# Optimization experiments

Measured on AMD Instinct MI355X. Metric: run time of the kernel, lower is better.

Reference implementation:

```python
import jax, jax.numpy as jnp
import numpy as np

B, N, D = 4, 2048, 512      # batch, seq, dim_in
DK = DV = 512               # dim_k == dim_v (required by fc input width)
NH = 8
HK = DK // NH               # per-head dk == dv == 64
SCALE = 1.0 / np.sqrt(HK)
LN_EPS = 1e-5


def setup_inputs() -> dict:
    key = jax.random.key(0)
    ks = jax.random.split(key, 8)
    s = 0.02
    return {
        "x": jax.random.normal(ks[0], (B, N, D), dtype=jnp.float32),
        "Wq": jax.random.normal(ks[1], (D, DK), dtype=jnp.float32) * s,
        "Wk": jax.random.normal(ks[2], (D, DK), dtype=jnp.float32) * s,
        "Wv": jax.random.normal(ks[3], (D, DV), dtype=jnp.float32) * s,
        "Wf": jax.random.normal(ks[4], (2 * DK, D), dtype=jnp.float32) * s,
        "bf": jnp.zeros((D,), dtype=jnp.float32),
        "gamma": jnp.ones((D,), dtype=jnp.float32),
        "beta": jnp.zeros((D,), dtype=jnp.float32),
    }


def reference(x, Wq, Wk, Wv, Wf, bf, gamma, beta):
    b, n, _ = x.shape
    # projections -> [b, nh, n, hk]; q_c/q_f etc. are identical in the source,
    # so compute once.
    def proj(W):
        return jnp.einsum('bnd,dk->bnk', x, W).reshape(b, n, NH, -1).transpose(0, 2, 1, 3)
    q, k, v = proj(Wq), proj(Wk), proj(Wv)

    # conventional branch: softmax over n x n scores
    dist_c = jax.nn.softmax(jnp.einsum('bhqd,bhkd->bhqk', q, k) * SCALE, axis=-1)
    att_c = jnp.einsum('bhqk,bhkd->bhqd', dist_c, v)          # [b,nh,n,hk]
    att_c = att_c.transpose(0, 2, 1, 3).reshape(b, n, DV)

    # feature branch: softmax over dk x dk scores (linear-complexity variant)
    dist_f = jax.nn.softmax(jnp.einsum('bhnk,bhnq->bhkq', k, q) * SCALE, axis=-1)
    att_f = jnp.einsum('bhnd,bhdq->bhnq', v, dist_f)           # [b,nh,n,hk]
    att_f = att_f.transpose(0, 2, 1, 3).reshape(b, n, DV)

    att = jnp.concatenate([att_c, att_f], axis=2)              # [b,n,2*dk]
    out = jax.nn.relu(att @ Wf + bf)                           # dropout=eval (identity)
    out = out + x
    mu = jnp.mean(out, axis=-1, keepdims=True)
    var = jnp.var(out, axis=-1, keepdims=True)
    out = (out - mu) * jax.lax.rsqrt(var + LN_EPS) * gamma + beta
    return out
```

## Files before the change

### kernel.cpp

```cpp
#include <hip/hip_runtime.h>
#include <math.h>
#include <stdint.h>

#define B_   4
#define N_   2048
#define D_   512
#define DK_  512
#define NH_  8
#define HK_  64
#define LN_EPS_ 1e-5f
#define QS_  0.18033688011112042f

typedef unsigned short u16;
typedef __attribute__((ext_vector_type(8))) short short8;
typedef __attribute__((ext_vector_type(4))) float f32x4;
typedef __attribute__((ext_vector_type(8))) unsigned short u16x8;

__device__ __forceinline__ u16 f2bf(float x) {
    uint32_t u = __builtin_bit_cast(uint32_t, x);
    return (u16)((u + 0x7fffu + ((u >> 16) & 1u)) >> 16);
}
__device__ __forceinline__ u16 f2bf_fast(float x) {
    return (u16)((__builtin_bit_cast(uint32_t, x) + 0x8000u) >> 16);
}
__device__ __forceinline__ float b2f(u16 v) {
    return __builtin_bit_cast(float, (uint32_t)v << 16);
}
__device__ __forceinline__ uint32_t cvtpk_bf16(float lo, float hi) {
    uint32_t r;
    asm("v_cvt_pk_bf16_f32 %0, %1, %2" : "=v"(r) : "v"(lo), "v"(hi));
    return r;
}
__device__ __forceinline__ float exp2f_fast(float x) {
    return __builtin_amdgcn_exp2f(x);
}

__device__ __forceinline__ void gload16(const void* g, void* l) {
    __builtin_amdgcn_global_load_lds(
        reinterpret_cast<const __attribute__((address_space(1))) void*>(
            reinterpret_cast<uintptr_t>(g)),
        reinterpret_cast<__attribute__((address_space(3))) void*>(
            static_cast<uint32_t>(reinterpret_cast<uintptr_t>(l))),
        16, 0, 0);
}

__global__ __launch_bounds__(256) void prep_kernel(
    const float* __restrict__ x, const float* __restrict__ Wq,
    const float* __restrict__ Wk, const float* __restrict__ Wv,
    const float* __restrict__ Wf, u16* __restrict__ xb,
    u16* __restrict__ wqkvT, u16* __restrict__ wfT)
{
    __shared__ float t[32][33];
    const int bid = blockIdx.x, tid = threadIdx.x;
    if (bid < 2048) {
        const int i = (bid * 256 + tid) * 8;
        const float4 a = *reinterpret_cast<const float4*>(&x[i]);
        const float4 b = *reinterpret_cast<const float4*>(&x[i + 4]);
        u16x8 o;
        o[0] = f2bf(a.x); o[1] = f2bf(a.y); o[2] = f2bf(a.z); o[3] = f2bf(a.w);
        o[4] = f2bf(b.x); o[5] = f2bf(b.y); o[6] = f2bf(b.z); o[7] = f2bf(b.w);
        *reinterpret_cast<u16x8*>(&xb[i]) = o;
        return;
    }
    const float* W;
    u16* dst;
    int K, Nc, nt, kt;
    if (bid < 2816) {
        const int z = (bid - 2048) >> 8, rem = (bid - 2048) & 255;
        W = z == 0 ? Wq : (z == 1 ? Wk : Wv);
        dst = wqkvT + (size_t)z * 512 * 512;
        K = 512; Nc = 512;
        nt = (rem & 15) * 32; kt = (rem >> 4) * 32;
    } else {
        const int rem = bid - 2816;
        W = Wf; dst = wfT; K = 1024; Nc = 512;
        nt = (rem & 15) * 32; kt = (rem >> 4) * 32;
    }
    {
        const int r = tid >> 3, c0 = (tid & 7) * 4;
        const float4 v = *reinterpret_cast<const float4*>(
            &W[(size_t)(kt + r) * Nc + nt + c0]);
        t[r][c0] = v.x; t[r][c0 + 1] = v.y; t[r][c0 + 2] = v.z; t[r][c0 + 3] = v.w;
    }
    __syncthreads();
    {
        const int nidx = tid >> 3, kc = (tid & 7) * 4;
        u16 o[4];
        #pragma unroll
        for (int j = 0; j < 4; ++j) o[j] = f2bf(t[kc + j][nidx]);
        *reinterpret_cast<ushort4*>(&dst[(size_t)(nt + nidx) * K + kt + kc]) =
            make_ushort4(o[0], o[1], o[2], o[3]);
    }
}

__global__ __launch_bounds__(256) void gemm_qkv_kernel(
    const u16* __restrict__ A, const u16* __restrict__ Bt,
    u16* __restrict__ qb, u16* __restrict__ kb,
    u16* __restrict__ vb, u16* __restrict__ vt)
{
    __shared__ u16 As0[64 * 64], As1[64 * 64];
    __shared__ u16 Bs0[128 * 64], Bs1[128 * 64];
    const int tid = threadIdx.x;
    const int lane = tid & 63, wave = tid >> 6;
    const int wm = wave >> 1, wn = wave & 1;
    const int l15 = lane & 15, lg = lane >> 4;
    const int bid = ((int)blockIdx.x & 7) * 192 + ((int)blockIdx.x >> 3);
    const int nt = (bid % 12) * 128;
    const int mt = (bid / 12) * 64;

    f32x4 acc[2][4] = {};

#define QKV_STAGE(kt, AS, BS) do {                                             \
    _Pragma("unroll")                                                          \
    for (int i_ = 0; i_ < 2; ++i_) {                                           \
        const int ob_ = (wave * 2 + i_) * 1024;                                \
        const int o_ = ob_ + lane * 16;                                        \
        const int row_ = o_ >> 7;                                              \
        const int inner_ = (o_ & 127) ^ ((row_ & 7) << 4);                     \
        gload16((const char*)A + ((size_t)(mt + row_) * 512 + (kt) * 64) * 2   \
                    + inner_, (char*)(AS) + ob_);                              \
    }                                                                          \
    _Pragma("unroll")                                                          \
    for (int i_ = 0; i_ < 4; ++i_) {                                           \
        const int ob_ = (wave * 4 + i_) * 1024;                                \
        const int o_ = ob_ + lane * 16;                                        \
        const int row_ = o_ >> 7;                                              \
        const int inner_ = (o_ & 127) ^ ((row_ & 7) << 4);                     \
        gload16((const char*)Bt + ((size_t)(nt + row_) * 512 + (kt) * 64) * 2  \
                    + inner_, (char*)(BS) + ob_);                              \
    }                                                                          \
} while (0)

#define QKV_COMP(AS, BS) do {                                                  \
    _Pragma("unroll")                                                          \
    for (int ks = 0; ks < 2; ++ks) {                                           \
        const int kb2 = ks * 32 + lg * 8;                                      \
        short8 af[2], bfr[4];                                                  \
        _Pragma("unroll")                                                      \
        for (int mi = 0; mi < 2; ++mi) {                                       \
            const int r = wm * 32 + mi * 16 + l15;                             \
            af[mi] = *reinterpret_cast<const short8*>(                         \
                &(AS)[r * 64 + (kb2 ^ ((r & 7) << 3))]);                       \
        }                                                                      \
        _Pragma("unroll")                                                      \
        for (int ni = 0; ni < 4; ++ni) {                                       \
            const int r = wn * 64 + ni * 16 + l15;                             \
            bfr[ni] = *reinterpret_cast<const short8*>(                        \
                &(BS)[r * 64 + (kb2 ^ ((r & 7) << 3))]);                       \
        }                                                                      \
        _Pragma("unroll")                                                      \
        for (int mi = 0; mi < 2; ++mi)                                         \
            _Pragma("unroll")                                                  \
            for (int ni = 0; ni < 4; ++ni)                                     \
                acc[mi][ni] = __builtin_amdgcn_mfma_f32_16x16x32_bf16(         \
                    af[mi], bfr[ni], acc[mi][ni], 0, 0, 0);                    \
    }                                                                          \
} while (0)

    QKV_STAGE(0, As0, Bs0);
    __syncthreads();
    #pragma unroll 1
    for (int kt = 0; kt < 8; kt += 2) {
        QKV_STAGE(kt + 1, As1, Bs1);
        QKV_COMP(As0, Bs0);
        __syncthreads();
        if (kt + 2 < 8) QKV_STAGE(kt + 2, As0, Bs0);
        QKV_COMP(As1, Bs1);
        __syncthreads();
    }
#undef QKV_STAGE
#undef QKV_COMP

    #pragma unroll
    for (int mi = 0; mi < 2; ++mi) {
        #pragma unroll
        for (int ni = 0; ni < 4; ++ni) {
            const int col = nt + wn * 64 + ni * 16 + l15;
            const int row0 = mt + wm * 32 + mi * 16 + lg * 4;
            if (col < 512) {
                #pragma unroll
                for (int jj = 0; jj < 4; ++jj)
                    qb[(size_t)(row0 + jj) * 512 + col] =
                        f2bf(acc[mi][ni][jj] * QS_);
            } else if (col < 1024) {
                #pragma unroll
                for (int jj = 0; jj < 4; ++jj)
                    kb[(size_t)(row0 + jj) * 512 + col - 512] =
                        f2bf(acc[mi][ni][jj]);
            } else {
                const int dfull = col - 1024;
                const int hh = dfull >> 6, dd = dfull & 63;
                const int bb = row0 >> 11, nn = row0 & 2047;
                u16 o4[4];
                #pragma unroll
                for (int jj = 0; jj < 4; ++jj) {
                    o4[jj] = f2bf(acc[mi][ni][jj]);
                    vb[(size_t)(row0 + jj) * 512 + dfull] = o4[jj];
                }
                *reinterpret_cast<ushort4*>(
                    &vt[(((size_t)(bb * NH_ + hh)) * HK_ + dd) * N_ + nn]) =
                    make_ushort4(o4[0], o4[1], o4[2], o4[3]);
            }
        }
    }
}

__global__ __launch_bounds__(256) void gemm_fc_kernel(
    const u16* __restrict__ A, const u16* __restrict__ Bt,
    u16* __restrict__ C, const float* __restrict__ bias,
    const float* __restrict__ resid)
{
    __shared__ u16 As0[64 * 64], As1[64 * 64];
    __shared__ u16 Bs0[128 * 64], Bs1[128 * 64];
    const int tid = threadIdx.x;
    const int lane = tid & 63, wave = tid >> 6;
    const int wm = wave >> 1, wn = wave & 1;
    const int l15 = lane & 15, lg = lane >> 4;
    const int bid = ((int)blockIdx.x & 7) * 64 + ((int)blockIdx.x >> 3);
    const int nt = (bid & 3) * 128;
    const int mt = (bid >> 2) * 64;

    f32x4 acc[2][4] = {};

#define FC_STAGE(kt, AS, BS) do {                                              \
    _Pragma("unroll")                                                          \
    for (int i_ = 0; i_ < 2; ++i_) {                                           \
        const int ob_ = (wave * 2 + i_) * 1024;                                \
        const int o_ = ob_ + lane * 16;                                        \
        const int row_ = o_ >> 7;                                              \
        const int inner_ = (o_ & 127) ^ ((row_ & 7) << 4);                     \
        gload16((const char*)A + ((size_t)(mt + row_) * 1024 + (kt) * 64) * 2  \
                    + inner_, (char*)(AS) + ob_);                              \
    }                                                                          \
    _Pragma("unroll")                                                          \
    for (int i_ = 0; i_ < 4; ++i_) {                                           \
        const int ob_ = (wave * 4 + i_) * 1024;                                \
        const int o_ = ob_ + lane * 16;                                        \
        const int row_ = o_ >> 7;                                              \
        const int inner_ = (o_ & 127) ^ ((row_ & 7) << 4);                     \
        gload16((const char*)Bt + ((size_t)(nt + row_) * 1024 + (kt) * 64) * 2 \
                    + inner_, (char*)(BS) + ob_);                              \
    }                                                                          \
} while (0)

#define FC_COMP(AS, BS) do {                                                   \
    _Pragma("unroll")                                                          \
    for (int ks = 0; ks < 2; ++ks) {                                           \
        const int kb2 = ks * 32 + lg * 8;                                      \
        short8 af[2], bfr[4];                                                  \
        _Pragma("unroll")                                                      \
        for (int mi = 0; mi < 2; ++mi) {                                       \
            const int r = wm * 32 + mi * 16 + l15;                             \
            af[mi] = *reinterpret_cast<const short8*>(                         \
                &(AS)[r * 64 + (kb2 ^ ((r & 7) << 3))]);                       \
        }                                                                      \
        _Pragma("unroll")                                                      \
        for (int ni = 0; ni < 4; ++ni) {                                       \
            const int r = wn * 64 + ni * 16 + l15;                             \
            bfr[ni] = *reinterpret_cast<const short8*>(                        \
                &(BS)[r * 64 + (kb2 ^ ((r & 7) << 3))]);                       \
        }                                                                      \
        _Pragma("unroll")                                                      \
        for (int mi = 0; mi < 2; ++mi)                                         \
            _Pragma("unroll")                                                  \
            for (int ni = 0; ni < 4; ++ni)                                     \
                acc[mi][ni] = __builtin_amdgcn_mfma_f32_16x16x32_bf16(         \
                    af[mi], bfr[ni], acc[mi][ni], 0, 0, 0);                    \
    }                                                                          \
} while (0)

    FC_STAGE(0, As0, Bs0);
    __syncthreads();
    #pragma unroll 1
    for (int kt = 0; kt < 16; kt += 2) {
        FC_STAGE(kt + 1, As1, Bs1);
        FC_COMP(As0, Bs0);
        __syncthreads();
        if (kt + 2 < 16) FC_STAGE(kt + 2, As0, Bs0);
        FC_COMP(As1, Bs1);
        __syncthreads();
    }
#undef FC_STAGE
#undef FC_COMP

    #pragma unroll
    for (int mi = 0; mi < 2; ++mi) {
        #pragma unroll
        for (int ni = 0; ni < 4; ++ni) {
            const int col = nt + wn * 64 + ni * 16 + l15;
            const int row0 = mt + wm * 32 + mi * 16 + lg * 4;
            #pragma unroll
            for (int jj = 0; jj < 4; ++jj) {
                const size_t row = (size_t)(row0 + jj);
                float v = acc[mi][ni][jj];
                v += bias[col];
                v = fmaxf(v, 0.0f);
                v += resid[row * 512 + col];
                C[row * 512 + col] = f2bf(v);
            }
        }
    }
}

__global__ __launch_bounds__(256) void flash_featS_kernel(
    const u16* __restrict__ Qb, const u16* __restrict__ Kb,
    const u16* __restrict__ Vt, u16* __restrict__ att,
    float* __restrict__ partials)
{
    __shared__ u16 sh[24576];
    const int tid = threadIdx.x;
    const int lane = tid & 63, wave = tid >> 6;
    const int l15 = lane & 15, lg = lane >> 4;

    if ((int)blockIdx.x >= 512) {
        u16* KsT = sh;
        u16* QsT = sh + 4096;
        const int fid = (int)blockIdx.x - 512;
        const int ns = fid & 7, h = (fid >> 3) & 7, b = fid >> 6;
        const size_t hbase = (size_t)b * N_ * DK_ + (size_t)h * HK_;

        f32x4 acc[4] = {};
        for (int c = 0; c < 4; ++c) {
            const int n0 = ns * 256 + c * 64;
            __syncthreads();
            #pragma unroll
            for (int it = 0; it < 2; ++it) {
                const int idx = tid + it * 256;
                const int n = idx >> 3, d0 = (idx & 7) * 8;
                const u16x8 kv = *reinterpret_cast<const u16x8*>(
                    &Kb[hbase + (size_t)(n0 + n) * DK_ + d0]);
                const u16x8 qv = *reinterpret_cast<const u16x8*>(
                    &Qb[hbase + (size_t)(n0 + n) * DK_ + d0]);
                #pragma unroll
                for (int j = 0; j < 8; ++j) {
                    const int r = d0 + j;
                    const int cidx = n ^ ((r & 7) << 3);
                    KsT[r * 64 + cidx] = kv[j];
                    QsT[r * 64 + cidx] = qv[j];
                }
            }
            __syncthreads();
            #pragma unroll
            for (int ks = 0; ks < 2; ++ks) {
                const int kb2 = ks * 32 + lg * 8;
                const int ar = wave * 16 + l15;
                const short8 aK = *reinterpret_cast<const short8*>(
                    &KsT[ar * 64 + (kb2 ^ ((ar & 7) << 3))]);
                #pragma unroll
                for (int ni = 0; ni < 4; ++ni) {
                    const int br = ni * 16 + l15;
                    const short8 bQ = *reinterpret_cast<const short8*>(
                        &QsT[br * 64 + (kb2 ^ ((br & 7) << 3))]);
                    acc[ni] = __builtin_amdgcn_mfma_f32_16x16x32_bf16(
                        aK, bQ, acc[ni], 0, 0, 0);
                }
            }
        }
        const int bh = b * NH_ + h;
        #pragma unroll
        for (int ni = 0; ni < 4; ++ni)
            #pragma unroll
            for (int jj = 0; jj < 4; ++jj) {
                const int row = wave * 16 + lg * 4 + jj;
                partials[(((size_t)ns * 32 + bh) * 64 + row) * 64 + ni * 16 + l15] =
                    acc[ni][jj];
            }
        return;
    }

    u16* kb0 = sh;
    u16* kb1 = sh + 4096;
    u16* vb0 = sh + 8192;
    u16* vb1 = sh + 12288;
    u16* Ps  = sh + 16384;
    const int lbid = (((int)blockIdx.x & 7) << 6) + ((int)blockIdx.x >> 3);
    const int qt = lbid & 15, h = (lbid >> 4) & 7, b = lbid >> 7;

    short8 aq[2][2];
    #pragma unroll
    for (int qs = 0; qs < 2; ++qs) {
        const int qrow = qt * 128 + qs * 64 + wave * 16 + l15;
        const u16* qp = Qb + ((size_t)(b * N_ + qrow)) * DK_ + h * HK_ + lg * 8;
        aq[qs][0] = *reinterpret_cast<const short8*>(qp);
        aq[qs][1] = *reinterpret_cast<const short8*>(qp + 32);
    }
    short8 ones;
    #pragma unroll
    for (int i = 0; i < 8; ++i) ones[i] = (short)0x3F80;

    const u16* Kbase = Kb + (size_t)b * N_ * DK_ + (size_t)h * HK_;
    const u16* Vbase = Vt + ((size_t)(b * NH_ + h)) * HK_ * N_;
    unsigned long long* Ps64 = reinterpret_cast<unsigned long long*>(Ps);

    f32x4 o[2][5] = {};
    float m_[2] = {-1e30f, -1e30f};
    f32x4 SA[2][4], SB[2][4];

    const int ob0 = wave * 1024, oo0 = ob0 + lane * 16;
    const int row0s = oo0 >> 7;
    const int in0 = (oo0 & 127) ^ ((row0s & 7) << 4);

#define STAGE_K(ktile, KBUF) do {                                              \
    gload16((const char*)Kbase +                                               \
                ((size_t)((ktile) * 64 + row0s) * DK_) * 2 + in0,              \
            (char*)(KBUF) + ob0);                                              \
    gload16((const char*)Kbase +                                               \
                ((size_t)((ktile) * 64 + 32 + row0s) * DK_) * 2 + in0,         \
            (char*)(KBUF) + 4096 + ob0);                                       \
} while (0)

#define STAGE_V(ktile, VBUF) do {                                              \
    gload16((const char*)Vbase +                                               \
                ((size_t)row0s * N_ + (ktile) * 64) * 2 + in0,                 \
            (char*)(VBUF) + ob0);                                              \
    gload16((const char*)Vbase +                                               \
                ((size_t)(32 + row0s) * N_ + (ktile) * 64) * 2 + in0,          \
            (char*)(VBUF) + 4096 + ob0);                                       \
} while (0)

#define QK_STEP(S, KBUF) do {                                                  \
    _Pragma("unroll")                                                          \
    for (int qs = 0; qs < 2; ++qs)                                             \
        _Pragma("unroll")                                                      \
        for (int t = 0; t < 4; ++t)                                            \
            S[qs][t] = (f32x4){0.0f, 0.0f, 0.0f, 0.0f};                        \
    __builtin_amdgcn_s_setprio(1);                                             \
    _Pragma("unroll")                                                          \
    for (int ks = 0; ks < 2; ++ks) {                                           \
        const int kb2 = ks * 32 + lg * 8;                                      \
        _Pragma("unroll")                                                      \
        for (int t = 0; t < 4; ++t) {                                          \
            const int r = t * 16 + l15;                                        \
            const short8 bk = *reinterpret_cast<const short8*>(                \
                &(KBUF)[r * 64 + (kb2 ^ ((r & 7) << 3))]);                     \
            S[0][t] = __builtin_amdgcn_mfma_f32_16x16x32_bf16(                 \
                bk, aq[0][ks], S[0][t], 0, 0, 0);                              \
            S[1][t] = __builtin_amdgcn_mfma_f32_16x16x32_bf16(                 \
                bk, aq[1][ks], S[1][t], 0, 0, 0);                              \
        }                                                                      \
    }                                                                          \
    __builtin_amdgcn_s_setprio(0);                                             \
} while (0)

#define SMPV_STEP(S, VBUF) do {                                                \
    float rmax[2], cm;                                                         \
    _Pragma("unroll")                                                          \
    for (int qs = 0; qs < 2; ++qs) {                                           \
        float a0 = fmaxf(fmaxf(S[qs][0][0], S[qs][0][1]),                      \
                         fmaxf(S[qs][0][2], S[qs][0][3]));                     \
        float a1 = fmaxf(fmaxf(S[qs][1][0], S[qs][1][1]),                      \
                         fmaxf(S[qs][1][2], S[qs][1][3]));                     \
        float a2 = fmaxf(fmaxf(S[qs][2][0], S[qs][2][1]),                      \
                         fmaxf(S[qs][2][2], S[qs][2][3]));                     \
        float a3 = fmaxf(fmaxf(S[qs][3][0], S[qs][3][1]),                      \
                         fmaxf(S[qs][3][2], S[qs][3][3]));                     \
        rmax[qs] = fmaxf(fmaxf(a0, a1), fmaxf(a2, a3));                        \
    }                                                                          \
    cm = fmaxf(rmax[0] - m_[0], rmax[1] - m_[1]);                              \
    if (__any(cm > 8.0f)) {                                                    \
        _Pragma("unroll")                                                      \
        for (int qs = 0; qs < 2; ++qs) {                                       \
            float rm = rmax[qs];                                               \
            rm = fmaxf(rm, __shfl_xor(rm, 16));                                \
            rm = fmaxf(rm, __shfl_xor(rm, 32));                                \
            const float newm = fmaxf(m_[qs], rm);                              \
            const float fac = exp2f_fast(m_[qs] - newm);                       \
            m_[qs] = newm;                                                     \
            float facq[4];                                                     \
            _Pragma("unroll")                                                  \
            for (int jj = 0; jj < 4; ++jj)                                     \
                facq[jj] = __shfl(fac, lg * 4 + jj);                           \
            _Pragma("unroll")                                                  \
            for (int t = 0; t < 5; ++t)                                        \
                _Pragma("unroll")                                              \
                for (int jj = 0; jj < 4; ++jj)                                 \
                    o[qs][t][jj] *= facq[jj];                                  \
        }                                                                      \
    }                                                                          \
    _Pragma("unroll")                                                          \
    for (int qs = 0; qs < 2; ++qs) {                                           \
        const int prow = qs * 64 + wave * 16 + l15;                            \
        const int pb64 = prow * 16;                                            \
        const int sw1 = (prow & 7) << 1;                                       \
        _Pragma("unroll")                                                      \
        for (int t = 0; t < 4; ++t) {                                          \
            const float p0 = exp2f_fast(S[qs][t][0] - m_[qs]);                 \
            const float p1 = exp2f_fast(S[qs][t][1] - m_[qs]);                 \
            const float p2 = exp2f_fast(S[qs][t][2] - m_[qs]);                 \
            const float p3 = exp2f_fast(S[qs][t][3] - m_[qs]);                 \
            const uint32_t lo = cvtpk_bf16(p0, p1);                            \
            const uint32_t hi = cvtpk_bf16(p2, p3);                            \
            Ps64[pb64 + ((t * 4 + lg) ^ sw1)] =                                \
                (unsigned long long)lo | ((unsigned long long)hi << 32);       \
        }                                                                      \
    }                                                                          \
    __builtin_amdgcn_s_setprio(1);                                             \
    _Pragma("unroll")                                                          \
    for (int ks = 0; ks < 2; ++ks) {                                           \
        const int kb2 = ks * 32 + lg * 8;                                      \
        const int pr0 = wave * 16 + l15;                                       \
        const int pr1 = 64 + pr0;                                              \
        const short8 ap0 = *reinterpret_cast<const short8*>(                   \
            &Ps[pr0 * 64 + (kb2 ^ ((pr0 & 7) << 3))]);                         \
        const short8 ap1 = *reinterpret_cast<const short8*>(                   \
            &Ps[pr1 * 64 + (kb2 ^ ((pr1 & 7) << 3))]);                         \
        _Pragma("unroll")                                                      \
        for (int t = 0; t < 4; ++t) {                                          \
            const int dr = t * 16 + l15;                                       \
            const short8 bv = *reinterpret_cast<const short8*>(                \
                &(VBUF)[dr * 64 + (kb2 ^ ((dr & 7) << 3))]);                   \
            o[0][t] = __builtin_amdgcn_mfma_f32_16x16x32_bf16(                 \
                ap0, bv, o[0][t], 0, 0, 0);                                    \
            o[1][t] = __builtin_amdgcn_mfma_f32_16x16x32_bf16(                 \
                ap1, bv, o[1][t], 0, 0, 0);                                    \
        }                                                                      \
        o[0][4] = __builtin_amdgcn_mfma_f32_16x16x32_bf16(                     \
            ap0, ones, o[0][4], 0, 0, 0);                                      \
        o[1][4] = __builtin_amdgcn_mfma_f32_16x16x32_bf16(                     \
            ap1, ones, o[1][4], 0, 0, 0);                                      \
    }                                                                          \
    __builtin_amdgcn_s_setprio(0);                                             \
} while (0)

    STAGE_K(0, kb0);
    STAGE_K(1, kb1);
    STAGE_V(0, vb0);
    __syncthreads();
    QK_STEP(SA, kb0);

    #pragma unroll 1
    for (int t2 = 0; t2 < 30; t2 += 2) {
        __syncthreads();
        STAGE_K(t2 + 2, kb0);
        STAGE_V(t2 + 1, vb1);
        QK_STEP(SB, kb1);
        SMPV_STEP(SA, vb0);
        __syncthreads();
        STAGE_K(t2 + 3, kb1);
        STAGE_V(t2 + 2, vb0);
        QK_STEP(SA, kb0);
        SMPV_STEP(SB, vb1);
    }
    __syncthreads();
    STAGE_V(31, vb1);
    QK_STEP(SB, kb1);
    SMPV_STEP(SA, vb0);
    __syncthreads();
    SMPV_STEP(SB, vb1);

#undef STAGE_K
#undef STAGE_V
#undef QK_STEP
#undef SMPV_STEP

    #pragma unroll
    for (int qs = 0; qs < 2; ++qs)
        #pragma unroll
        for (int jj = 0; jj < 4; ++jj) {
            const float inv = 1.0f / o[qs][4][jj];
            const size_t row = (size_t)b * N_ + qt * 128 + qs * 64 + wave * 16 + lg * 4 + jj;
            #pragma unroll
            for (int t = 0; t < 4; ++t)
                att[row * (2 * DK_) + h * HK_ + t * 16 + l15] =
                    f2bf_fast(o[qs][t][jj] * inv);
        }
}

__global__ __launch_bounds__(256) void featSM_kernel(
    const float* __restrict__ partials, u16* __restrict__ distfT)
{
    const int bh = blockIdx.x, rg = blockIdx.y, tid = threadIdx.x;
    const int r = rg * 16 + (tid >> 4);
    const int tl = tid & 15;
    float v[4] = {0.0f, 0.0f, 0.0f, 0.0f};
    for (int s = 0; s < 8; ++s) {
        const float4 a = *reinterpret_cast<const float4*>(
            &partials[(((size_t)s * 32 + bh) * 64 + r) * 64 + tl * 4]);
        v[0] += a.x; v[1] += a.y; v[2] += a.z; v[3] += a.w;
    }
    float m = fmaxf(fmaxf(v[0], v[1]), fmaxf(v[2], v[3]));
    m = fmaxf(m, __shfl_xor(m, 1));
    m = fmaxf(m, __shfl_xor(m, 2));
    m = fmaxf(m, __shfl_xor(m, 4));
    m = fmaxf(m, __shfl_xor(m, 8));
    float sum = 0.0f;
    #pragma unroll
    for (int j = 0; j < 4; ++j) { v[j] = exp2f_fast(v[j] - m); sum += v[j]; }
    sum += __shfl_xor(sum, 1);
    sum += __shfl_xor(sum, 2);
    sum += __shfl_xor(sum, 4);
    sum += __shfl_xor(sum, 8);
    const float inv = 1.0f / sum;
    #pragma unroll
    for (int j = 0; j < 4; ++j)
        distfT[(size_t)bh * 4096 + (tl * 4 + j) * 64 + r] = f2bf_fast(v[j] * inv);
}

__global__ __launch_bounds__(256) void featAV_mfma(
    const u16* __restrict__ V, const u16* __restrict__ distfT,
    u16* __restrict__ att)
{
    __shared__ u16 Bs[64 * 64];
    __shared__ u16 As[64 * 64];
    const int tid = threadIdx.x;
    const int lane = tid & 63, wave = tid >> 6;
    const int l15 = lane & 15, lg = lane >> 4;
    const int ns = blockIdx.x, h = blockIdx.y, b = blockIdx.z;
    const int bh = b * NH_ + h;
    const int n0 = ns * 64;

    #pragma unroll
    for (int it = 0; it < 2; ++it) {
        const int idx = tid + it * 256;
        const int r = idx >> 3, c0 = (idx & 7) * 8;
        const u16x8 dv = *reinterpret_cast<const u16x8*>(
            &distfT[(size_t)bh * 4096 + r * 64 + c0]);
        *reinterpret_cast<u16x8*>(&Bs[r * 64 + (c0 ^ ((r & 7) << 3))]) = dv;
    }
    #pragma unroll
    for (int i = 0; i < 2; ++i) {
        const int ob = (wave * 2 + i) * 1024;
        const int o_ = ob + lane * 16;
        const int row = o_ >> 7;
        const int inner = (o_ & 127) ^ ((row & 7) << 4);
        gload16((const char*)V + ((size_t)(b * N_ + n0 + row) * DK_ + h * HK_) * 2 + inner,
                (char*)As + ob);
    }
    __syncthreads();
    f32x4 acc[4] = {};
    #pragma unroll
    for (int ks = 0; ks < 2; ++ks) {
        const int kb2 = ks * 32 + lg * 8;
        const int ar = wave * 16 + l15;
        const short8 av = *reinterpret_cast<const short8*>(
            &As[ar * 64 + (kb2 ^ ((ar & 7) << 3))]);
        #pragma unroll
        for (int ni = 0; ni < 4; ++ni) {
            const int br = ni * 16 + l15;
            const short8 bd = *reinterpret_cast<const short8*>(
                &Bs[br * 64 + (kb2 ^ ((br & 7) << 3))]);
            acc[ni] = __builtin_amdgcn_mfma_f32_16x16x32_bf16(av, bd, acc[ni], 0, 0, 0);
        }
    }
    #pragma unroll
    for (int ni = 0; ni < 4; ++ni)
        #pragma unroll
        for (int jj = 0; jj < 4; ++jj)
            att[((size_t)b * N_ + n0 + wave * 16 + lg * 4 + jj) * (2 * DK_)
                + 512 + h * HK_ + ni * 16 + l15] = f2bf_fast(acc[ni][jj]);
}

__global__ __launch_bounds__(256) void ln_kernel(
    const u16* __restrict__ fc, const float* __restrict__ gamma,
    const float* __restrict__ beta, float* __restrict__ out)
{
    const int row = blockIdx.x * 4 + (threadIdx.x >> 6);
    const int lane = threadIdx.x & 63;
    const int c = lane * 8;
    const u16x8 v = *reinterpret_cast<const u16x8*>(&fc[(size_t)row * D_ + c]);
    float f[8];
    float s = 0.0f, sq = 0.0f;
    #pragma unroll
    for (int j = 0; j < 8; ++j) {
        f[j] = b2f(v[j]);
        s += f[j];
        sq = fmaf(f[j], f[j], sq);
    }
    #pragma unroll
    for (int off = 32; off >= 1; off >>= 1) {
        s  += __shfl_xor(s, off);
        sq += __shfl_xor(sq, off);
    }
    const float mu = s * (1.0f / D_);
    const float var = sq * (1.0f / D_) - mu * mu;
    const float rstd = rsqrtf(var + LN_EPS_);
    const float4 g0 = *reinterpret_cast<const float4*>(&gamma[c]);
    const float4 g1 = *reinterpret_cast<const float4*>(&gamma[c + 4]);
    const float4 b0 = *reinterpret_cast<const float4*>(&beta[c]);
    const float4 b1 = *reinterpret_cast<const float4*>(&beta[c + 4]);
    const float gg[8] = {g0.x, g0.y, g0.z, g0.w, g1.x, g1.y, g1.z, g1.w};
    const float bb[8] = {b0.x, b0.y, b0.z, b0.w, b1.x, b1.y, b1.z, b1.w};
    float4 o0, o1;
    o0.x = (f[0] - mu) * rstd * gg[0] + bb[0];
    o0.y = (f[1] - mu) * rstd * gg[1] + bb[1];
    o0.z = (f[2] - mu) * rstd * gg[2] + bb[2];
    o0.w = (f[3] - mu) * rstd * gg[3] + bb[3];
    o1.x = (f[4] - mu) * rstd * gg[4] + bb[4];
    o1.y = (f[5] - mu) * rstd * gg[5] + bb[5];
    o1.z = (f[6] - mu) * rstd * gg[6] + bb[6];
    o1.w = (f[7] - mu) * rstd * gg[7] + bb[7];
    *reinterpret_cast<float4*>(&out[(size_t)row * D_ + c]) = o0;
    *reinterpret_cast<float4*>(&out[(size_t)row * D_ + c + 4]) = o1;
}

extern "C" void kernel_launch(void* const* d_in, const int* in_sizes, int n_in,
                              void* d_out, int out_size, void* d_ws, size_t ws_size,
                              hipStream_t stream)
{
    (void)in_sizes; (void)n_in; (void)out_size; (void)ws_size;
    const float* x     = (const float*)d_in[0];
    const float* Wq    = (const float*)d_in[1];
    const float* Wk    = (const float*)d_in[2];
    const float* Wv    = (const float*)d_in[3];
    const float* Wf    = (const float*)d_in[4];
    const float* bf    = (const float*)d_in[5];
    const float* gamma = (const float*)d_in[6];
    const float* beta  = (const float*)d_in[7];
    float* out = (float*)d_out;

    char* w = (char*)d_ws;
    const size_t SZE = (size_t)B_ * N_ * DK_;
    u16* xb     = (u16*)w;   w += SZE * 2;
    u16* wqkvT  = (u16*)w;   w += (size_t)1536 * 512 * 2;
    u16* wfT    = (u16*)w;   w += (size_t)512 * 1024 * 2;
    u16* qb     = (u16*)w;   w += SZE * 2;
    u16* kb     = (u16*)w;   w += SZE * 2;
    u16* vb     = (u16*)w;   w += SZE * 2;
    u16* vt     = (u16*)w;   w += SZE * 2;
    u16* attb   = (u16*)w;   w += SZE * 2 * 2;
    float* partials = (float*)w; w += (size_t)8 * 32 * 4096 * 4;
    u16* distfT = (u16*)w;   w += (size_t)32 * 4096 * 2;
    u16* fcout  = (u16*)w;

    const dim3 blk(256);

    prep_kernel<<<dim3(3328), blk, 0, stream>>>(x, Wq, Wk, Wv, Wf, xb, wqkvT, wfT);

    gemm_qkv_kernel<<<dim3(1536), blk, 0, stream>>>(xb, wqkvT, qb, kb, vb, vt);

    flash_featS_kernel<<<dim3(768), blk, 0, stream>>>(qb, kb, vt, attb, partials);

    featSM_kernel<<<dim3(32, 4), blk, 0, stream>>>(partials, distfT);
    featAV_mfma<<<dim3(32, NH_, B_), blk, 0, stream>>>(vb, distfT, attb);

    gemm_fc_kernel<<<dim3(512), blk, 0, stream>>>(attb, wfT, fcout, bf, x);

    ln_kernel<<<dim3(2048), blk, 0, stream>>>(fcout, gamma, beta, out);
}
```

Baseline: 116.3 us.

## Fuse x fp32-to-bf16 conversion into QKV GEMM and move Wf transpose into flash kernel

The QKV GEMM now loads fp32 x directly through registers, converts it to bf16 and writes it into swizzled LDS, so the separate x conversion pass and the xb buffer go away. The Wf transpose/convert blocks move out of the prep kernel and become extra blocks in the flash_featS launch, which shrinks prep to the QKV weight transposes only. This removes a full write and re-read of x in bf16, but the GEMM A operand now reads twice as many bytes through register-staged loads instead of direct global-to-LDS loads, and the conversion adds ALU work in the GEMM loop.

```diff
diff --git a/kernel.cpp b/kernel.cpp
--- a/kernel.cpp
+++ b/kernel.cpp
@@ -45,41 +45,19 @@
 }
 
 __global__ __launch_bounds__(256) void prep_kernel(
-    const float* __restrict__ x, const float* __restrict__ Wq,
-    const float* __restrict__ Wk, const float* __restrict__ Wv,
-    const float* __restrict__ Wf, u16* __restrict__ xb,
-    u16* __restrict__ wqkvT, u16* __restrict__ wfT)
+    const float* __restrict__ Wq, const float* __restrict__ Wk,
+    const float* __restrict__ Wv, u16* __restrict__ wqkvT)
 {
     __shared__ float t[32][33];
     const int bid = blockIdx.x, tid = threadIdx.x;
-    if (bid < 2048) {
-        const int i = (bid * 256 + tid) * 8;
-        const float4 a = *reinterpret_cast<const float4*>(&x[i]);
-        const float4 b = *reinterpret_cast<const float4*>(&x[i + 4]);
-        u16x8 o;
-        o[0] = f2bf(a.x); o[1] = f2bf(a.y); o[2] = f2bf(a.z); o[3] = f2bf(a.w);
-        o[4] = f2bf(b.x); o[5] = f2bf(b.y); o[6] = f2bf(b.z); o[7] = f2bf(b.w);
-        *reinterpret_cast<u16x8*>(&xb[i]) = o;
-        return;
-    }
-    const float* W;
-    u16* dst;
-    int K, Nc, nt, kt;
-    if (bid < 2816) {
-        const int z = (bid - 2048) >> 8, rem = (bid - 2048) & 255;
-        W = z == 0 ? Wq : (z == 1 ? Wk : Wv);
-        dst = wqkvT + (size_t)z * 512 * 512;
-        K = 512; Nc = 512;
-        nt = (rem & 15) * 32; kt = (rem >> 4) * 32;
-    } else {
-        const int rem = bid - 2816;
-        W = Wf; dst = wfT; K = 1024; Nc = 512;
-        nt = (rem & 15) * 32; kt = (rem >> 4) * 32;
-    }
+    const int z = bid >> 8, rem = bid & 255;
+    const float* W = z == 0 ? Wq : (z == 1 ? Wk : Wv);
+    u16* dst = wqkvT + (size_t)z * 512 * 512;
+    const int nt = (rem & 15) * 32, kt = (rem >> 4) * 32;
     {
         const int r = tid >> 3, c0 = (tid & 7) * 4;
         const float4 v = *reinterpret_cast<const float4*>(
-            &W[(size_t)(kt + r) * Nc + nt + c0]);
+            &W[(size_t)(kt + r) * 512 + nt + c0]);
         t[r][c0] = v.x; t[r][c0 + 1] = v.y; t[r][c0 + 2] = v.z; t[r][c0 + 3] = v.w;
     }
     __syncthreads();
@@ -88,13 +66,13 @@
         u16 o[4];
         #pragma unroll
         for (int j = 0; j < 4; ++j) o[j] = f2bf(t[kc + j][nidx]);
-        *reinterpret_cast<ushort4*>(&dst[(size_t)(nt + nidx) * K + kt + kc]) =
+        *reinterpret_cast<ushort4*>(&dst[(size_t)(nt + nidx) * 512 + kt + kc]) =
             make_ushort4(o[0], o[1], o[2], o[3]);
     }
 }
 
 __global__ __launch_bounds__(256) void gemm_qkv_kernel(
-    const u16* __restrict__ A, const u16* __restrict__ Bt,
+    const float* __restrict__ X, const u16* __restrict__ Bt,
     u16* __restrict__ qb, u16* __restrict__ kb,
     u16* __restrict__ vb, u16* __restrict__ vt)
 {
@@ -108,18 +86,38 @@
     const int nt = (bid % 12) * 128;
     const int mt = (bid / 12) * 64;
 
+    const int ar_ = tid >> 2;
+    const int ac0_ = (tid & 3) * 16;
+    const int aswz_ = (ar_ & 7) << 4;
+    float4 al0, al1, al2, al3;
+
     f32x4 acc[2][4] = {};
 
-#define QKV_STAGE(kt, AS, BS) do {                                             \
-    _Pragma("unroll")                                                          \
-    for (int i_ = 0; i_ < 2; ++i_) {                                           \
-        const int ob_ = (wave * 2 + i_) * 1024;                                \
-        const int o_ = ob_ + lane * 16;                                        \
-        const int row_ = o_ >> 7;                                              \
-        const int inner_ = (o_ & 127) ^ ((row_ & 7) << 4);                     \
-        gload16((const char*)A + ((size_t)(mt + row_) * 512 + (kt) * 64) * 2   \
-                    + inner_, (char*)(AS) + ob_);                              \
-    }                                                                          \
+#define A_LOAD(kt) do {                                                        \
+    const float* xp_ = &X[(size_t)(mt + ar_) * 512 + (kt) * 64 + ac0_];        \
+    al0 = *reinterpret_cast<const float4*>(xp_);                               \
+    al1 = *reinterpret_cast<const float4*>(xp_ + 4);                           \
+    al2 = *reinterpret_cast<const float4*>(xp_ + 8);                           \
+    al3 = *reinterpret_cast<const float4*>(xp_ + 12);                          \
+} while (0)
+
+#define A_WRITE(AS) do {                                                       \
+    u16x8 w0_, w1_;                                                            \
+    w0_[0] = f2bf(al0.x); w0_[1] = f2bf(al0.y);                                \
+    w0_[2] = f2bf(al0.z); w0_[3] = f2bf(al0.w);                                \
+    w0_[4] = f2bf(al1.x); w0_[5] = f2bf(al1.y);                                \
+    w0_[6] = f2bf(al1.z); w0_[7] = f2bf(al1.w);                                \
+    w1_[0] = f2bf(al2.x); w1_[1] = f2bf(al2.y);                                \
+    w1_[2] = f2bf(al2.z); w1_[3] = f2bf(al2.w);                                \
+    w1_[4] = f2bf(al3.x); w1_[5] = f2bf(al3.y);                                \
+    w1_[6] = f2bf(al3.z); w1_[7] = f2bf(al3.w);                                \
+    *reinterpret_cast<u16x8*>((char*)(AS) + ar_ * 128 +                        \
+                              ((2 * ac0_) ^ aswz_)) = w0_;                     \
+    *reinterpret_cast<u16x8*>((char*)(AS) + ar_ * 128 +                        \
+                              ((2 * ac0_ + 16) ^ aswz_)) = w1_;                \
+} while (0)
+
+#define B_STAGE(kt, BS) do {                                                   \
     _Pragma("unroll")                                                          \
     for (int i_ = 0; i_ < 4; ++i_) {                                           \
         const int ob_ = (wave * 4 + i_) * 1024;                                \
@@ -157,18 +155,22 @@
     }                                                                          \
 } while (0)
 
-    QKV_STAGE(0, As0, Bs0);
+    A_LOAD(0); B_STAGE(0, Bs0); A_WRITE(As0);
     __syncthreads();
     #pragma unroll 1
     for (int kt = 0; kt < 8; kt += 2) {
-        QKV_STAGE(kt + 1, As1, Bs1);
+        A_LOAD(kt + 1); B_STAGE(kt + 1, Bs1);
         QKV_COMP(As0, Bs0);
+        A_WRITE(As1);
         __syncthreads();
-        if (kt + 2 < 8) QKV_STAGE(kt + 2, As0, Bs0);
+        if (kt + 2 < 8) { A_LOAD(kt + 2); B_STAGE(kt + 2, Bs0); }
         QKV_COMP(As1, Bs1);
+        if (kt + 2 < 8) A_WRITE(As0);
         __syncthreads();
     }
-#undef QKV_STAGE
+#undef A_LOAD
+#undef A_WRITE
+#undef B_STAGE
 #undef QKV_COMP
 
     #pragma unroll
@@ -305,12 +307,36 @@
 __global__ __launch_bounds__(256) void flash_featS_kernel(
     const u16* __restrict__ Qb, const u16* __restrict__ Kb,
     const u16* __restrict__ Vt, u16* __restrict__ att,
-    float* __restrict__ partials)
+    float* __restrict__ partials,
+    const float* __restrict__ Wf, u16* __restrict__ wfT)
 {
     __shared__ u16 sh[24576];
     const int tid = threadIdx.x;
     const int lane = tid & 63, wave = tid >> 6;
     const int l15 = lane & 15, lg = lane >> 4;
+
+    if ((int)blockIdx.x >= 768) {
+        float* t = reinterpret_cast<float*>(sh);
+        const int rem = (int)blockIdx.x - 768;
+        const int nt = (rem & 15) * 32, kt = (rem >> 4) * 32;
+        {
+            const int r = tid >> 3, c0 = (tid & 7) * 4;
+            const float4 v = *reinterpret_cast<const float4*>(
+                &Wf[(size_t)(kt + r) * 512 + nt + c0]);
+            t[r * 33 + c0] = v.x; t[r * 33 + c0 + 1] = v.y;
+            t[r * 33 + c0 + 2] = v.z; t[r * 33 + c0 + 3] = v.w;
+        }
+        __syncthreads();
+        {
+            const int nidx = tid >> 3, kc = (tid & 7) * 4;
+            u16 o[4];
+            #pragma unroll
+            for (int j = 0; j < 4; ++j) o[j] = f2bf(t[(kc + j) * 33 + nidx]);
+            *reinterpret_cast<ushort4*>(&wfT[(size_t)(nt + nidx) * 1024 + kt + kc]) =
+                make_ushort4(o[0], o[1], o[2], o[3]);
+        }
+        return;
+    }
 
     if ((int)blockIdx.x >= 512) {
         u16* KsT = sh;
@@ -710,7 +736,6 @@
 
     char* w = (char*)d_ws;
     const size_t SZE = (size_t)B_ * N_ * DK_;
-    u16* xb     = (u16*)w;   w += SZE * 2;
     u16* wqkvT  = (u16*)w;   w += (size_t)1536 * 512 * 2;
     u16* wfT    = (u16*)w;   w += (size_t)512 * 1024 * 2;
     u16* qb     = (u16*)w;   w += SZE * 2;
@@ -724,11 +749,12 @@
 
     const dim3 blk(256);
 
-    prep_kernel<<<dim3(3328), blk, 0, stream>>>(x, Wq, Wk, Wv, Wf, xb, wqkvT, wfT);
-
-    gemm_qkv_kernel<<<dim3(1536), blk, 0, stream>>>(xb, wqkvT, qb, kb, vb, vt);
-
-    flash_featS_kernel<<<dim3(768), blk, 0, stream>>>(qb, kb, vt, attb, partials);
+    prep_kernel<<<dim3(768), blk, 0, stream>>>(Wq, Wk, Wv, wqkvT);
+
+    gemm_qkv_kernel<<<dim3(1536), blk, 0, stream>>>(x, wqkvT, qb, kb, vb, vt);
+
+    flash_featS_kernel<<<dim3(1280), blk, 0, stream>>>(
+        qb, kb, vt, attb, partials, Wf, wfT);
 
     featSM_kernel<<<dim3(32, 4), blk, 0, stream>>>(partials, distfT);
     featAV_mfma<<<dim3(32, NH_, B_), blk, 0, stream>>>(vb, distfT, attb);
```

New measurement: 120.0 us. 3.2% more time.
